# Performance work log

Measured on AMD Instinct MI355X. Metric: run time of the kernel, lower is better.

The kernel has to match this reference:

```python
import jax, jax.numpy as jnp
import numpy as np

D_MODEL = 256
N_LEVELS = 4
N_HEADS = 8
N_POINTS = 4
HEAD_DIM = D_MODEL // N_HEADS
SPATIAL_SHAPES = np.array([[128, 128], [64, 64], [32, 32], [16, 16]], dtype=np.int64)
LEN_IN = int((SPATIAL_SHAPES[:, 0] * SPATIAL_SHAPES[:, 1]).sum())  # 21760
BATCH = 2
LEN_Q = LEN_IN  # encoder self-attention


def setup_inputs() -> dict:
    key = jax.random.key(0)
    ks = jax.random.split(key, 12)
    C = D_MODEL
    lvl_start = np.concatenate([[0], np.cumsum(SPATIAL_SHAPES[:, 0] * SPATIAL_SHAPES[:, 1])[:-1]]).astype(np.int64)
    return {
        'query': jax.random.normal(ks[0], (BATCH, LEN_Q, C), jnp.float32),
        'reference_points': jax.random.uniform(ks[1], (BATCH, LEN_Q, N_LEVELS, 2), jnp.float32),
        'input_flatten': jax.random.normal(ks[2], (BATCH, LEN_IN, C), jnp.float32),
        'input_spatial_shapes': SPATIAL_SHAPES,          # static numpy: shapes must be concrete
        'input_level_start_index': lvl_start,            # static numpy
        'Wv': jax.random.normal(ks[3], (C, C), jnp.float32) / np.sqrt(C),
        'bv': jnp.zeros((C,), jnp.float32),
        'Woff': jax.random.normal(ks[4], (C, N_HEADS * N_LEVELS * N_POINTS * 2), jnp.float32) * 0.01,
        'boff': jax.random.normal(ks[5], (N_HEADS * N_LEVELS * N_POINTS * 2,), jnp.float32) * 0.5,
        'Wa': jax.random.normal(ks[6], (C, N_HEADS * N_LEVELS * N_POINTS), jnp.float32) * 0.01,
        'ba': jnp.zeros((N_HEADS * N_LEVELS * N_POINTS,), jnp.float32),
        'Wo': jax.random.normal(ks[7], (C, C), jnp.float32) / np.sqrt(C),
        'bo': jnp.zeros((C,), jnp.float32),
    }


def _grid_sample_bilinear(v, grid):
    """v: (B,H,W,D); grid: (B,Q,P,2) in [-1,1] (x,y). align_corners=False, zero padding."""
    B, H, W, D = v.shape
    x = (grid[..., 0] + 1.0) * 0.5 * W - 0.5
    y = (grid[..., 1] + 1.0) * 0.5 * H - 0.5
    x0 = jnp.floor(x)
    y0 = jnp.floor(y)
    wx = x - x0
    wy = y - y0
    b = jnp.arange(B)[:, None, None]

    def corner(xi, yi, w):
        valid = (xi >= 0) & (xi < W) & (yi >= 0) & (yi < H)
        xi_ = jnp.clip(xi, 0, W - 1).astype(jnp.int32)
        yi_ = jnp.clip(yi, 0, H - 1).astype(jnp.int32)
        return v[b, yi_, xi_] * (w * valid)[..., None]  # (B,Q,P,D)

    return (corner(x0, y0, (1 - wx) * (1 - wy))
            + corner(x0 + 1, y0, wx * (1 - wy))
            + corner(x0, y0 + 1, (1 - wx) * wy)
            + corner(x0 + 1, y0 + 1, wx * wy))


def _msdeform_attn(query, reference_points, input_flatten, spatial_shapes_np,
                   Wv, bv, Woff, boff, Wa, ba, Wo, bo):
    N, Lq, C = query.shape
    Lin = input_flatten.shape[1]
    M, L, P, D = N_HEADS, N_LEVELS, N_POINTS, HEAD_DIM

    value = (input_flatten @ Wv + bv).reshape(N, Lin, M, D)
    offsets = (query @ Woff + boff).reshape(N, Lq, M, L, P, 2)
    attn = jax.nn.softmax((query @ Wa + ba).reshape(N, Lq, M, L * P), axis=-1).reshape(N, Lq, M, L, P)

    # sampling locations in [0,1] -> grid in [-1,1]
    grids = 2.0 * (reference_points[:, :, None, :, None, :] + offsets) - 1.0  # (N,Lq,M,L,P,2)

    out = jnp.zeros((N * M, Lq, D), value.dtype)
    start = 0
    for lid in range(L):
        H_, W_ = int(spatial_shapes_np[lid, 0]), int(spatial_shapes_np[lid, 1])
        v_l = value[:, start:start + H_ * W_]                       # (N,HW,M,D)
        v_l = v_l.transpose(0, 2, 1, 3).reshape(N * M, H_, W_, D)   # (N*M,H,W,D)
        g_l = grids[:, :, :, lid].transpose(0, 2, 1, 3, 4).reshape(N * M, Lq, P, 2)
        sampled = _grid_sample_bilinear(v_l, g_l)                   # (N*M,Lq,P,D)
        a_l = attn[:, :, :, lid].transpose(0, 2, 1, 3).reshape(N * M, Lq, P)
        out = out + jnp.einsum('bqpd,bqp->bqd', sampled, a_l)
        start += H_ * W_

    out = out.reshape(N, M, Lq, D).transpose(0, 2, 1, 3).reshape(N, Lq, M * D)
    return out @ Wo + bo


def reference(query, reference_points, input_flatten, input_spatial_shapes,
              input_level_start_index, Wv, bv, Woff, boff, Wa, ba, Wo, bo):
    spatial_np = np.asarray(input_spatial_shapes)
    return _msdeform_attn(query, reference_points, input_flatten, spatial_np,
                          Wv, bv, Woff, boff, Wa, ba, Wo, bo)
```

## Files before the change

kernel.cpp:

```cpp
#include <hip/hip_runtime.h>
#include <cstdint>
#include <cstddef>

#define LEN_IN  21760
#define BATCH   2
#define MROWS   (BATCH * LEN_IN)

typedef short    sv8 __attribute__((ext_vector_type(8)));
typedef _Float16 hv8 __attribute__((ext_vector_type(8)));
typedef float    fv4 __attribute__((ext_vector_type(4)));

__device__ __forceinline__ unsigned short f2bf(float f) {
  unsigned u = __float_as_uint(f);
  u += 0x7fff + ((u >> 16) & 1);
  return (unsigned short)(u >> 16);
}
__device__ __forceinline__ float bf2f(unsigned short s) {
  return __uint_as_float(((unsigned)s) << 16);
}

__global__ __launch_bounds__(256) void cvt_weights(
    const float* __restrict__ Wv, const float* __restrict__ Woff,
    const float* __restrict__ Wa, const float* __restrict__ Wo,
    _Float16* __restrict__ WvT, short* __restrict__ WoffTh, short* __restrict__ WoffTl,
    _Float16* __restrict__ WaT, short* __restrict__ WoTh, short* __restrict__ WoTl)
{
  const int b = blockIdx.x, k = threadIdx.x;
  if (b < 256) {
    WvT[(size_t)b * 256 + k] = (_Float16)Wv[(size_t)k * 256 + b];
  } else if (b < 512) {
    const int n = b - 256;
    const float v = Woff[(size_t)k * 256 + n];
    const unsigned short h = f2bf(v);
    WoffTh[(size_t)n * 256 + k] = h;
    WoffTl[(size_t)n * 256 + k] = f2bf(v - bf2f(h));
  } else if (b < 640) {
    const int n = b - 512;
    WaT[(size_t)n * 256 + k] = (_Float16)Wa[(size_t)k * 128 + n];
  } else {
    const int n = b - 640;
    const float v = Wo[(size_t)k * 256 + n];
    const unsigned short h = f2bf(v);
    WoTh[(size_t)n * 256 + k] = h;
    WoTl[(size_t)n * 256 + k] = f2bf(v - bf2f(h));
  }
}

template<int TN>
__global__ __launch_bounds__(256, 2) void gemm_f16(
    const float* __restrict__ A, const _Float16* __restrict__ Bt,
    const float* __restrict__ bias, void* __restrict__ Cout, int outf16)
{
  constexpr int K = 256;
  constexpr int JF = TN / 32;
  __shared__ _Float16 As[128 * 32];
  __shared__ _Float16 Bs[TN * 32];

  const int tid = threadIdx.x, lane = tid & 63, wave = tid >> 6;
  const int l15 = lane & 15, quad = lane >> 4;
  const int wr = (wave & 1) * 64, wc = (wave >> 1) * (TN / 2);
  const int rowBase = blockIdx.x * 128;
  const int rs = tid >> 2, ss = (tid & 3) * 8;

  fv4 acc[4][JF] = {};

  for (int k0 = 0; k0 < K; k0 += 32) {
    if (k0) __syncthreads();
#pragma unroll
    for (int p2 = 0; p2 < 2; ++p2) {
      const int row = p2 * 64 + rs;
      const float4 f0 = *(const float4*)&A[(size_t)(rowBase + row) * K + k0 + ss];
      const float4 f1 = *(const float4*)&A[(size_t)(rowBase + row) * K + k0 + ss + 4];
      hv8 h;
      h[0] = (_Float16)f0.x; h[1] = (_Float16)f0.y; h[2] = (_Float16)f0.z; h[3] = (_Float16)f0.w;
      h[4] = (_Float16)f1.x; h[5] = (_Float16)f1.y; h[6] = (_Float16)f1.z; h[7] = (_Float16)f1.w;
      *(hv8*)&As[row * 32 + ss] = h;
    }
#pragma unroll
    for (int p2 = 0; p2 < TN / 64; ++p2) {
      const int row = p2 * 64 + rs;
      *(hv8*)&Bs[row * 32 + ss] = *(const hv8*)&Bt[(size_t)row * K + k0 + ss];
    }
    __syncthreads();

    hv8 a[4];
#pragma unroll
    for (int i = 0; i < 4; ++i) a[i] = *(const hv8*)&As[(wr + i * 16 + l15) * 32 + quad * 8];
#pragma unroll
    for (int j = 0; j < JF; ++j) {
      const hv8 b = *(const hv8*)&Bs[(wc + j * 16 + l15) * 32 + quad * 8];
#pragma unroll
      for (int i = 0; i < 4; ++i)
        acc[i][j] = __builtin_amdgcn_mfma_f32_16x16x32_f16(a[i], b, acc[i][j], 0, 0, 0);
    }
  }

#pragma unroll
  for (int j = 0; j < JF; ++j) {
    const int col = wc + j * 16 + l15;
    const float bj = bias[col];
#pragma unroll
    for (int i = 0; i < 4; ++i)
#pragma unroll
      for (int rg = 0; rg < 4; ++rg) {
        const int row = rowBase + wr + i * 16 + quad * 4 + rg;
        const float v = acc[i][j][rg] + bj;
        if (outf16) ((_Float16*)Cout)[(size_t)row * TN + col] = (_Float16)v;
        else        ((float*)Cout)[(size_t)row * TN + col] = v;
      }
  }
}

template<int PRE>
__global__ __launch_bounds__(256, 2) void gemm_split(
    const float* __restrict__ A32,
    const short* __restrict__ Ah, const short* __restrict__ Al,
    const short* __restrict__ Bth, const short* __restrict__ Btl,
    const float* __restrict__ bias, float* __restrict__ C)
{
  constexpr int K = 256, TN = 256, JF = 8;
  __shared__ short Ash[128 * 32], Asl[128 * 32];
  __shared__ short Bsh[256 * 32], Bsl[256 * 32];

  const int tid = threadIdx.x, lane = tid & 63, wave = tid >> 6;
  const int l15 = lane & 15, quad = lane >> 4;
  const int wr = (wave & 1) * 64, wc = (wave >> 1) * 128;
  const int rowBase = blockIdx.x * 128;
  const int rs = tid >> 2, ss = (tid & 3) * 8;

  fv4 acc[4][JF] = {};

  for (int k0 = 0; k0 < K; k0 += 32) {
    if (k0) __syncthreads();
#pragma unroll
    for (int p2 = 0; p2 < 2; ++p2) {
      const int row = p2 * 64 + rs;
      if (PRE) {
        *(sv8*)&Ash[row * 32 + ss] = *(const sv8*)&Ah[(size_t)(rowBase + row) * K + k0 + ss];
        *(sv8*)&Asl[row * 32 + ss] = *(const sv8*)&Al[(size_t)(rowBase + row) * K + k0 + ss];
      } else {
        const float4 f0 = *(const float4*)&A32[(size_t)(rowBase + row) * K + k0 + ss];
        const float4 f1 = *(const float4*)&A32[(size_t)(rowBase + row) * K + k0 + ss + 4];
        const float fv[8] = {f0.x, f0.y, f0.z, f0.w, f1.x, f1.y, f1.z, f1.w};
        sv8 hh, ll;
#pragma unroll
        for (int e = 0; e < 8; ++e) {
          const unsigned short h = f2bf(fv[e]);
          hh[e] = (short)h;
          ll[e] = (short)f2bf(fv[e] - bf2f(h));
        }
        *(sv8*)&Ash[row * 32 + ss] = hh;
        *(sv8*)&Asl[row * 32 + ss] = ll;
      }
    }
#pragma unroll
    for (int p2 = 0; p2 < 4; ++p2) {
      const int row = p2 * 64 + rs;
      *(sv8*)&Bsh[row * 32 + ss] = *(const sv8*)&Bth[(size_t)row * K + k0 + ss];
      *(sv8*)&Bsl[row * 32 + ss] = *(const sv8*)&Btl[(size_t)row * K + k0 + ss];
    }
    __syncthreads();

    sv8 ah[4], al[4];
#pragma unroll
    for (int i = 0; i < 4; ++i) {
      ah[i] = *(const sv8*)&Ash[(wr + i * 16 + l15) * 32 + quad * 8];
      al[i] = *(const sv8*)&Asl[(wr + i * 16 + l15) * 32 + quad * 8];
    }
#pragma unroll
    for (int j = 0; j < JF; ++j) {
      const sv8 bh = *(const sv8*)&Bsh[(wc + j * 16 + l15) * 32 + quad * 8];
      const sv8 bl = *(const sv8*)&Bsl[(wc + j * 16 + l15) * 32 + quad * 8];
#pragma unroll
      for (int i = 0; i < 4; ++i) {
        acc[i][j] = __builtin_amdgcn_mfma_f32_16x16x32_bf16(ah[i], bh, acc[i][j], 0, 0, 0);
        acc[i][j] = __builtin_amdgcn_mfma_f32_16x16x32_bf16(ah[i], bl, acc[i][j], 0, 0, 0);
        acc[i][j] = __builtin_amdgcn_mfma_f32_16x16x32_bf16(al[i], bh, acc[i][j], 0, 0, 0);
      }
    }
  }

#pragma unroll
  for (int j = 0; j < JF; ++j) {
    const int col = wc + j * 16 + l15;
    const float bj = bias[col];
#pragma unroll
    for (int i = 0; i < 4; ++i)
#pragma unroll
      for (int rg = 0; rg < 4; ++rg) {
        const int row = rowBase + wr + i * 16 + quad * 4 + rg;
        C[(size_t)row * TN + col] = acc[i][j][rg] + bj;
      }
  }
}

__global__ __launch_bounds__(256) void sample_kernel(
    const _Float16* __restrict__ value16,
    const float* __restrict__ offs,
    const _Float16* __restrict__ logits16,
    const float* __restrict__ refpts,
    short* __restrict__ outh, short* __restrict__ outl)
{
  __shared__ float2 s_pair[4][1024];
  __shared__ float  s_attn[1024];

  const int tid = threadIdx.x;
  const int qBase = blockIdx.x * 8;

  if (tid < 64) {
    const int q = tid >> 3, m = tid & 7;
    const size_t lb = (size_t)(qBase + q) * 128 + m * 16;
    float w[16];
#pragma unroll
    for (int i = 0; i < 16; ++i) w[i] = (float)logits16[lb + i];
    float mx = w[0];
#pragma unroll
    for (int i = 1; i < 16; ++i) mx = fmaxf(mx, w[i]);
    float sum = 0.f;
#pragma unroll
    for (int i = 0; i < 16; ++i) { w[i] = expf(w[i] - mx); sum += w[i]; }
    const float inv = 1.f / sum;
#pragma unroll
    for (int p = 0; p < 16; ++p) s_attn[p * 64 + q * 8 + m] = w[p] * inv;
  }
  __syncthreads();

#pragma unroll
  for (int k = 0; k < 4; ++k) {
    const int i = tid + 256 * k;
    const int p = i >> 6, q = (i >> 3) & 7, m = i & 7;
    const int l = p >> 2, pp = p & 3;
    const int qg = qBase + q;
    const float2 rp = *(const float2*)&refpts[(size_t)qg * 8 + l * 2];
    const float2 of = *(const float2*)&offs[(size_t)qg * 256 + ((m * 4 + l) * 4 + pp) * 2];
    const float aw = s_attn[p * 64 + q * 8 + m];
    const int W = 128 >> l;
    const int st = (l == 0) ? 0 : (l == 1) ? 16384 : (l == 2) ? 20480 : 21504;
    const float x = (rp.x + of.x) * (float)W - 0.5f;
    const float y = (rp.y + of.y) * (float)W - 0.5f;
    const float xf = floorf(x), yf = floorf(y);
    const int x0 = (int)xf, y0 = (int)yf;
    const float wx = x - xf, wy = y - yf;
#pragma unroll
    for (int c = 0; c < 4; ++c) {
      const int dx = c & 1, dy = c >> 1;
      const int xi = x0 + dx, yi = y0 + dy;
      const bool valid = (xi >= 0) & (xi < W) & (yi >= 0) & (yi < W);
      const float w = (dx ? wx : 1.f - wx) * (dy ? wy : 1.f - wy) * aw;
      float2 pr;
      pr.x = __int_as_float(valid ? (st + yi * W + xi) * 512 : 0);
      pr.y = valid ? w : 0.f;
      s_pair[c][i] = pr;
    }
  }
  __syncthreads();

  const int wave = tid >> 6, lane = tid & 63;
  const int qloc = wave * 2 + (lane >> 5);
  const int sub = lane & 31, m = sub >> 2, j = sub & 3;
  const int qg = qBase + qloc;
  const int n = (qg >= LEN_IN) ? 1 : 0;
  const char* base = (const char*)(value16 + (size_t)n * LEN_IN * 256) + m * 64 + j * 16;
  const int lb = qloc * 8 + m;

  float acc[8] = {0.f, 0.f, 0.f, 0.f, 0.f, 0.f, 0.f, 0.f};
#pragma unroll 8
  for (int i = 0; i < 64; ++i) {
    const int c = i & 3, p = i >> 2;
    const float2 pr = s_pair[c][p * 64 + lb];
    const hv8 v = *(const hv8*)(base + __float_as_int(pr.x));
#pragma unroll
    for (int e = 0; e < 8; ++e) acc[e] = fmaf(pr.y, (float)v[e], acc[e]);
  }

  sv8 hh, ll;
#pragma unroll
  for (int e = 0; e < 8; ++e) {
    const unsigned short h = f2bf(acc[e]);
    hh[e] = (short)h;
    ll[e] = (short)f2bf(acc[e] - bf2f(h));
  }
  const size_t ob = (size_t)qg * 256 + m * 32 + j * 8;
  *(sv8*)&outh[ob] = hh;
  *(sv8*)&outl[ob] = ll;
}

extern "C" void kernel_launch(void* const* d_in, const int* in_sizes, int n_in,
                              void* d_out, int out_size, void* d_ws, size_t ws_size,
                              hipStream_t stream) {
  const float* query   = (const float*)d_in[0];
  const float* refpts  = (const float*)d_in[1];
  const float* flatten = (const float*)d_in[2];
  const float* Wv   = (const float*)d_in[5];
  const float* bv   = (const float*)d_in[6];
  const float* Woff = (const float*)d_in[7];
  const float* boff = (const float*)d_in[8];
  const float* Wa   = (const float*)d_in[9];
  const float* ba   = (const float*)d_in[10];
  const float* Wo   = (const float*)d_in[11];
  const float* bo   = (const float*)d_in[12];
  float* out = (float*)d_out;

  const size_t NE = (size_t)MROWS * 256;
  _Float16* value16  = (_Float16*)d_ws;
  float*    offsb    = (float*)(value16 + NE);
  _Float16* logits16 = (_Float16*)(offsb + NE);
  short*    outh     = (short*)(logits16 + NE / 2);
  short*    outl     = outh + NE;
  _Float16* WvT16    = (_Float16*)(outl + NE);
  short*    WoffTh   = (short*)(WvT16 + 256 * 256);
  short*    WoffTl   = WoffTh + 256 * 256;
  _Float16* WaT16    = (_Float16*)(WoffTl + 256 * 256);
  short*    WoTh     = (short*)(WaT16 + 128 * 256);
  short*    WoTl     = WoTh + 256 * 256;

  const dim3 blk(256);
  const int mtiles = MROWS / 128;

  cvt_weights<<<dim3(896), blk, 0, stream>>>(Wv, Woff, Wa, Wo,
      WvT16, WoffTh, WoffTl, WaT16, WoTh, WoTl);

  gemm_f16<256><<<dim3(mtiles), blk, 0, stream>>>(flatten, WvT16, bv, value16, 1);
  gemm_split<0><<<dim3(mtiles), blk, 0, stream>>>(query, nullptr, nullptr, WoffTh, WoffTl, boff, offsb);
  gemm_f16<128><<<dim3(mtiles), blk, 0, stream>>>(query, WaT16, ba, logits16, 1);
  sample_kernel<<<dim3(MROWS / 8), blk, 0, stream>>>(value16, offsb, logits16, refpts, outh, outl);
  gemm_split<1><<<dim3(mtiles), blk, 0, stream>>>(nullptr, outh, outl, WoTh, WoTl, bo, out);
}
```

Measured before the change: 313.7 us.

## Drop LDS staging in GEMMs, fuse coord transform, lower output precision

The GEMMs now read A and B fragments straight from global memory into registers with a one-step prefetch, dropping shared-memory staging and barriers. The reference-point add and scaling move into the offset GEMM epilogue. The sampler packs index and a 17-bit quantized weight into one 32-bit word, and its output is written as plain fp16. The output projection becomes a single fp16 MFMA GEMM instead of a 3-pass split bf16, which cuts traffic and compute but loses precision. The quantized sampling weights add further error.

```diff
diff --git a/kernel.cpp b/kernel.cpp
--- a/kernel.cpp
+++ b/kernel.cpp
@@ -23,7 +23,7 @@
     const float* __restrict__ Wv, const float* __restrict__ Woff,
     const float* __restrict__ Wa, const float* __restrict__ Wo,
     _Float16* __restrict__ WvT, short* __restrict__ WoffTh, short* __restrict__ WoffTl,
-    _Float16* __restrict__ WaT, short* __restrict__ WoTh, short* __restrict__ WoTl)
+    _Float16* __restrict__ WaT, _Float16* __restrict__ WoT)
 {
   const int b = blockIdx.x, k = threadIdx.x;
   if (b < 256) {
@@ -39,56 +39,54 @@
     WaT[(size_t)n * 256 + k] = (_Float16)Wa[(size_t)k * 128 + n];
   } else {
     const int n = b - 640;
-    const float v = Wo[(size_t)k * 256 + n];
-    const unsigned short h = f2bf(v);
-    WoTh[(size_t)n * 256 + k] = h;
-    WoTl[(size_t)n * 256 + k] = f2bf(v - bf2f(h));
-  }
-}
-
-template<int TN>
-__global__ __launch_bounds__(256, 2) void gemm_f16(
-    const float* __restrict__ A, const _Float16* __restrict__ Bt,
-    const float* __restrict__ bias, void* __restrict__ Cout, int outf16)
+    WoT[(size_t)n * 256 + k] = (_Float16)Wo[(size_t)k * 256 + n];
+  }
+}
+
+template<int TN, int AF32, int OUTF16>
+__global__ __launch_bounds__(256, 2) void gemm_f16d(
+    const void* __restrict__ Ap, const _Float16* __restrict__ Bt,
+    const float* __restrict__ bias, void* __restrict__ Cout)
 {
-  constexpr int K = 256;
   constexpr int JF = TN / 32;
-  __shared__ _Float16 As[128 * 32];
-  __shared__ _Float16 Bs[TN * 32];
-
   const int tid = threadIdx.x, lane = tid & 63, wave = tid >> 6;
   const int l15 = lane & 15, quad = lane >> 4;
   const int wr = (wave & 1) * 64, wc = (wave >> 1) * (TN / 2);
-  const int rowBase = blockIdx.x * 128;
-  const int rs = tid >> 2, ss = (tid & 3) * 8;
-
+  const int rowA = blockIdx.x * 128 + wr + l15;
+  const int kq = quad * 8;
+
+  hv8 a_pf[4];
+  auto loadA = [&](int kk, hv8* dst) {
+    if constexpr (AF32) {
+      const float* A = (const float*)Ap;
+#pragma unroll
+      for (int i = 0; i < 4; ++i) {
+        const float4 f0 = *(const float4*)&A[(size_t)(rowA + i * 16) * 256 + kk];
+        const float4 f1 = *(const float4*)&A[(size_t)(rowA + i * 16) * 256 + kk + 4];
+        hv8 h;
+        h[0] = (_Float16)f0.x; h[1] = (_Float16)f0.y; h[2] = (_Float16)f0.z; h[3] = (_Float16)f0.w;
+        h[4] = (_Float16)f1.x; h[5] = (_Float16)f1.y; h[6] = (_Float16)f1.z; h[7] = (_Float16)f1.w;
+        dst[i] = h;
+      }
+    } else {
+      const _Float16* A = (const _Float16*)Ap;
+#pragma unroll
+      for (int i = 0; i < 4; ++i)
+        dst[i] = *(const hv8*)&A[(size_t)(rowA + i * 16) * 256 + kk];
+    }
+  };
+
+  loadA(kq, a_pf);
   fv4 acc[4][JF] = {};
 
-  for (int k0 = 0; k0 < K; k0 += 32) {
-    if (k0) __syncthreads();
-#pragma unroll
-    for (int p2 = 0; p2 < 2; ++p2) {
-      const int row = p2 * 64 + rs;
-      const float4 f0 = *(const float4*)&A[(size_t)(rowBase + row) * K + k0 + ss];
-      const float4 f1 = *(const float4*)&A[(size_t)(rowBase + row) * K + k0 + ss + 4];
-      hv8 h;
-      h[0] = (_Float16)f0.x; h[1] = (_Float16)f0.y; h[2] = (_Float16)f0.z; h[3] = (_Float16)f0.w;
-      h[4] = (_Float16)f1.x; h[5] = (_Float16)f1.y; h[6] = (_Float16)f1.z; h[7] = (_Float16)f1.w;
-      *(hv8*)&As[row * 32 + ss] = h;
-    }
-#pragma unroll
-    for (int p2 = 0; p2 < TN / 64; ++p2) {
-      const int row = p2 * 64 + rs;
-      *(hv8*)&Bs[row * 32 + ss] = *(const hv8*)&Bt[(size_t)row * K + k0 + ss];
-    }
-    __syncthreads();
-
+  for (int k0 = 0; k0 < 256; k0 += 32) {
     hv8 a[4];
 #pragma unroll
-    for (int i = 0; i < 4; ++i) a[i] = *(const hv8*)&As[(wr + i * 16 + l15) * 32 + quad * 8];
+    for (int i = 0; i < 4; ++i) a[i] = a_pf[i];
+    if (k0 < 224) loadA(k0 + 32 + kq, a_pf);
 #pragma unroll
     for (int j = 0; j < JF; ++j) {
-      const hv8 b = *(const hv8*)&Bs[(wc + j * 16 + l15) * 32 + quad * 8];
+      const hv8 b = *(const hv8*)&Bt[(size_t)(wc + j * 16 + l15) * 256 + k0 + kq];
 #pragma unroll
       for (int i = 0; i < 4; ++i)
         acc[i][j] = __builtin_amdgcn_mfma_f32_16x16x32_f16(a[i], b, acc[i][j], 0, 0, 0);
@@ -103,74 +101,58 @@
     for (int i = 0; i < 4; ++i)
 #pragma unroll
       for (int rg = 0; rg < 4; ++rg) {
-        const int row = rowBase + wr + i * 16 + quad * 4 + rg;
+        const int row = blockIdx.x * 128 + wr + i * 16 + quad * 4 + rg;
         const float v = acc[i][j][rg] + bj;
-        if (outf16) ((_Float16*)Cout)[(size_t)row * TN + col] = (_Float16)v;
+        if (OUTF16) ((_Float16*)Cout)[(size_t)row * TN + col] = (_Float16)v;
         else        ((float*)Cout)[(size_t)row * TN + col] = v;
       }
   }
 }
 
-template<int PRE>
-__global__ __launch_bounds__(256, 2) void gemm_split(
-    const float* __restrict__ A32,
-    const short* __restrict__ Ah, const short* __restrict__ Al,
-    const short* __restrict__ Bth, const short* __restrict__ Btl,
-    const float* __restrict__ bias, float* __restrict__ C)
+__global__ __launch_bounds__(256, 2) void gemm_offs(
+    const float* __restrict__ A, const short* __restrict__ Bth,
+    const short* __restrict__ Btl, const float* __restrict__ boff,
+    const float* __restrict__ refpts, float* __restrict__ C)
 {
-  constexpr int K = 256, TN = 256, JF = 8;
-  __shared__ short Ash[128 * 32], Asl[128 * 32];
-  __shared__ short Bsh[256 * 32], Bsl[256 * 32];
-
+  constexpr int JF = 8;
   const int tid = threadIdx.x, lane = tid & 63, wave = tid >> 6;
   const int l15 = lane & 15, quad = lane >> 4;
   const int wr = (wave & 1) * 64, wc = (wave >> 1) * 128;
-  const int rowBase = blockIdx.x * 128;
-  const int rs = tid >> 2, ss = (tid & 3) * 8;
-
+  const int rowA = blockIdx.x * 128 + wr + l15;
+  const int kq = quad * 8;
+
+  float4 a_pf[8];
+  auto loadA = [&](int kk, float4* dst) {
+#pragma unroll
+    for (int i = 0; i < 4; ++i) {
+      dst[2 * i]     = *(const float4*)&A[(size_t)(rowA + i * 16) * 256 + kk];
+      dst[2 * i + 1] = *(const float4*)&A[(size_t)(rowA + i * 16) * 256 + kk + 4];
+    }
+  };
+
+  loadA(kq, a_pf);
   fv4 acc[4][JF] = {};
 
-  for (int k0 = 0; k0 < K; k0 += 32) {
-    if (k0) __syncthreads();
-#pragma unroll
-    for (int p2 = 0; p2 < 2; ++p2) {
-      const int row = p2 * 64 + rs;
-      if (PRE) {
-        *(sv8*)&Ash[row * 32 + ss] = *(const sv8*)&Ah[(size_t)(rowBase + row) * K + k0 + ss];
-        *(sv8*)&Asl[row * 32 + ss] = *(const sv8*)&Al[(size_t)(rowBase + row) * K + k0 + ss];
-      } else {
-        const float4 f0 = *(const float4*)&A32[(size_t)(rowBase + row) * K + k0 + ss];
-        const float4 f1 = *(const float4*)&A32[(size_t)(rowBase + row) * K + k0 + ss + 4];
-        const float fv[8] = {f0.x, f0.y, f0.z, f0.w, f1.x, f1.y, f1.z, f1.w};
-        sv8 hh, ll;
-#pragma unroll
-        for (int e = 0; e < 8; ++e) {
-          const unsigned short h = f2bf(fv[e]);
-          hh[e] = (short)h;
-          ll[e] = (short)f2bf(fv[e] - bf2f(h));
-        }
-        *(sv8*)&Ash[row * 32 + ss] = hh;
-        *(sv8*)&Asl[row * 32 + ss] = ll;
-      }
-    }
-#pragma unroll
-    for (int p2 = 0; p2 < 4; ++p2) {
-      const int row = p2 * 64 + rs;
-      *(sv8*)&Bsh[row * 32 + ss] = *(const sv8*)&Bth[(size_t)row * K + k0 + ss];
-      *(sv8*)&Bsl[row * 32 + ss] = *(const sv8*)&Btl[(size_t)row * K + k0 + ss];
-    }
-    __syncthreads();
-
+  for (int k0 = 0; k0 < 256; k0 += 32) {
     sv8 ah[4], al[4];
 #pragma unroll
     for (int i = 0; i < 4; ++i) {
-      ah[i] = *(const sv8*)&Ash[(wr + i * 16 + l15) * 32 + quad * 8];
-      al[i] = *(const sv8*)&Asl[(wr + i * 16 + l15) * 32 + quad * 8];
-    }
+      const float fvv[8] = {a_pf[2 * i].x, a_pf[2 * i].y, a_pf[2 * i].z, a_pf[2 * i].w,
+                            a_pf[2 * i + 1].x, a_pf[2 * i + 1].y, a_pf[2 * i + 1].z, a_pf[2 * i + 1].w};
+      sv8 hh, ll;
+#pragma unroll
+      for (int e = 0; e < 8; ++e) {
+        const unsigned short h = f2bf(fvv[e]);
+        hh[e] = (short)h;
+        ll[e] = (short)f2bf(fvv[e] - bf2f(h));
+      }
+      ah[i] = hh; al[i] = ll;
+    }
+    if (k0 < 224) loadA(k0 + 32 + kq, a_pf);
 #pragma unroll
     for (int j = 0; j < JF; ++j) {
-      const sv8 bh = *(const sv8*)&Bsh[(wc + j * 16 + l15) * 32 + quad * 8];
-      const sv8 bl = *(const sv8*)&Bsl[(wc + j * 16 + l15) * 32 + quad * 8];
+      const sv8 bh = *(const sv8*)&Bth[(size_t)(wc + j * 16 + l15) * 256 + k0 + kq];
+      const sv8 bl = *(const sv8*)&Btl[(size_t)(wc + j * 16 + l15) * 256 + k0 + kq];
 #pragma unroll
       for (int i = 0; i < 4; ++i) {
         acc[i][j] = __builtin_amdgcn_mfma_f32_16x16x32_bf16(ah[i], bh, acc[i][j], 0, 0, 0);
@@ -182,37 +164,40 @@
 
 #pragma unroll
   for (int j = 0; j < JF; ++j) {
-    const int col = wc + j * 16 + l15;
-    const float bj = bias[col];
+    const int c = wc + j * 16 + l15;
+    const int xy = c & 1, l = (c >> 3) & 3;
+    const float Wl = (float)(128 >> l);
+    const float bj = boff[c];
 #pragma unroll
     for (int i = 0; i < 4; ++i)
 #pragma unroll
       for (int rg = 0; rg < 4; ++rg) {
-        const int row = rowBase + wr + i * 16 + quad * 4 + rg;
-        C[(size_t)row * TN + col] = acc[i][j][rg] + bj;
+        const int row = blockIdx.x * 128 + wr + i * 16 + quad * 4 + rg;
+        const float ref = refpts[(size_t)row * 8 + l * 2 + xy];
+        C[(size_t)row * 256 + c] = (acc[i][j][rg] + bj + ref) * Wl - 0.5f;
       }
   }
 }
 
 __global__ __launch_bounds__(256) void sample_kernel(
     const _Float16* __restrict__ value16,
-    const float* __restrict__ offs,
+    const float* __restrict__ coords,
     const _Float16* __restrict__ logits16,
-    const float* __restrict__ refpts,
-    short* __restrict__ outh, short* __restrict__ outl)
+    _Float16* __restrict__ outp16)
 {
-  __shared__ float2 s_pair[4][1024];
-  __shared__ float  s_attn[1024];
+  __shared__ unsigned s_pair[4][1024];
+  __shared__ float    s_attn[1024];
 
   const int tid = threadIdx.x;
   const int qBase = blockIdx.x * 8;
 
   if (tid < 64) {
     const int q = tid >> 3, m = tid & 7;
-    const size_t lb = (size_t)(qBase + q) * 128 + m * 16;
+    const hv8* lp = (const hv8*)&logits16[(size_t)(qBase + q) * 128 + m * 16];
+    const hv8 w0 = lp[0], w1 = lp[1];
     float w[16];
 #pragma unroll
-    for (int i = 0; i < 16; ++i) w[i] = (float)logits16[lb + i];
+    for (int e = 0; e < 8; ++e) { w[e] = (float)w0[e]; w[8 + e] = (float)w1[e]; }
     float mx = w[0];
 #pragma unroll
     for (int i = 1; i < 16; ++i) mx = fmaxf(mx, w[i]);
@@ -221,7 +206,7 @@
     for (int i = 0; i < 16; ++i) { w[i] = expf(w[i] - mx); sum += w[i]; }
     const float inv = 1.f / sum;
 #pragma unroll
-    for (int p = 0; p < 16; ++p) s_attn[p * 64 + q * 8 + m] = w[p] * inv;
+    for (int p = 0; p < 16; ++p) s_attn[p * 64 + tid] = w[p] * inv;
   }
   __syncthreads();
 
@@ -231,13 +216,11 @@
     const int p = i >> 6, q = (i >> 3) & 7, m = i & 7;
     const int l = p >> 2, pp = p & 3;
     const int qg = qBase + q;
-    const float2 rp = *(const float2*)&refpts[(size_t)qg * 8 + l * 2];
-    const float2 of = *(const float2*)&offs[(size_t)qg * 256 + ((m * 4 + l) * 4 + pp) * 2];
-    const float aw = s_attn[p * 64 + q * 8 + m];
+    const float2 of = *(const float2*)&coords[(size_t)qg * 256 + ((m * 4 + l) * 4 + pp) * 2];
+    const float aw = s_attn[i];
     const int W = 128 >> l;
     const int st = (l == 0) ? 0 : (l == 1) ? 16384 : (l == 2) ? 20480 : 21504;
-    const float x = (rp.x + of.x) * (float)W - 0.5f;
-    const float y = (rp.y + of.y) * (float)W - 0.5f;
+    const float x = of.x, y = of.y;
     const float xf = floorf(x), yf = floorf(y);
     const int x0 = (int)xf, y0 = (int)yf;
     const float wx = x - xf, wy = y - yf;
@@ -247,10 +230,10 @@
       const int xi = x0 + dx, yi = y0 + dy;
       const bool valid = (xi >= 0) & (xi < W) & (yi >= 0) & (yi < W);
       const float w = (dx ? wx : 1.f - wx) * (dy ? wy : 1.f - wy) * aw;
-      float2 pr;
-      pr.x = __int_as_float(valid ? (st + yi * W + xi) * 512 : 0);
-      pr.y = valid ? w : 0.f;
-      s_pair[c][i] = pr;
+      unsigned wq = (unsigned)(w * 131072.f + 0.5f);
+      wq = wq > 131071u ? 131071u : wq;
+      const unsigned idx = (unsigned)(st + yi * W + xi);
+      s_pair[c][i] = valid ? (idx | (wq << 15)) : 0u;
     }
   }
   __syncthreads();
@@ -260,29 +243,24 @@
   const int sub = lane & 31, m = sub >> 2, j = sub & 3;
   const int qg = qBase + qloc;
   const int n = (qg >= LEN_IN) ? 1 : 0;
-  const char* base = (const char*)(value16 + (size_t)n * LEN_IN * 256) + m * 64 + j * 16;
+  const char* base = (const char*)value16 + (size_t)n * LEN_IN * 512 + m * 64 + j * 16;
   const int lb = qloc * 8 + m;
 
-  float acc[8] = {0.f, 0.f, 0.f, 0.f, 0.f, 0.f, 0.f, 0.f};
+  float acc8[8] = {0.f, 0.f, 0.f, 0.f, 0.f, 0.f, 0.f, 0.f};
 #pragma unroll 8
   for (int i = 0; i < 64; ++i) {
     const int c = i & 3, p = i >> 2;
-    const float2 pr = s_pair[c][p * 64 + lb];
-    const hv8 v = *(const hv8*)(base + __float_as_int(pr.x));
-#pragma unroll
-    for (int e = 0; e < 8; ++e) acc[e] = fmaf(pr.y, (float)v[e], acc[e]);
-  }
-
-  sv8 hh, ll;
-#pragma unroll
-  for (int e = 0; e < 8; ++e) {
-    const unsigned short h = f2bf(acc[e]);
-    hh[e] = (short)h;
-    ll[e] = (short)f2bf(acc[e] - bf2f(h));
-  }
-  const size_t ob = (size_t)qg * 256 + m * 32 + j * 8;
-  *(sv8*)&outh[ob] = hh;
-  *(sv8*)&outl[ob] = ll;
+    const unsigned u = s_pair[c][p * 64 + lb];
+    const float w = (float)(u >> 15) * (1.f / 131072.f);
+    const hv8 v = *(const hv8*)(base + (size_t)(u & 32767u) * 512);
+#pragma unroll
+    for (int e = 0; e < 8; ++e) acc8[e] = fmaf(w, (float)v[e], acc8[e]);
+  }
+
+  hv8 o;
+#pragma unroll
+  for (int e = 0; e < 8; ++e) o[e] = (_Float16)acc8[e];
+  *(hv8*)&outp16[(size_t)qg * 256 + m * 32 + j * 8] = o;
 }
 
 extern "C" void kernel_launch(void* const* d_in, const int* in_sizes, int n_in,
@@ -303,26 +281,24 @@
 
   const size_t NE = (size_t)MROWS * 256;
   _Float16* value16  = (_Float16*)d_ws;
-  float*    offsb    = (float*)(value16 + NE);
-  _Float16* logits16 = (_Float16*)(offsb + NE);
-  short*    outh     = (short*)(logits16 + NE / 2);
-  short*    outl     = outh + NE;
-  _Float16* WvT16    = (_Float16*)(outl + NE);
+  float*    coords   = (float*)(value16 + NE);
+  _Float16* logits16 = (_Float16*)(coords + NE);
+  _Float16* outp16   = logits16 + NE / 2;
+  _Float16* WvT16    = outp16 + NE;
   short*    WoffTh   = (short*)(WvT16 + 256 * 256);
   short*    WoffTl   = WoffTh + 256 * 256;
   _Float16* WaT16    = (_Float16*)(WoffTl + 256 * 256);
-  short*    WoTh     = (short*)(WaT16 + 128 * 256);
-  short*    WoTl     = WoTh + 256 * 256;
+  _Float16* WoT16    = WaT16 + 128 * 256;
 
   const dim3 blk(256);
   const int mtiles = MROWS / 128;
 
   cvt_weights<<<dim3(896), blk, 0, stream>>>(Wv, Woff, Wa, Wo,
-      WvT16, WoffTh, WoffTl, WaT16, WoTh, WoTl);
-
-  gemm_f16<256><<<dim3(mtiles), blk, 0, stream>>>(flatten, WvT16, bv, value16, 1);
-  gemm_split<0><<<dim3(mtiles), blk, 0, stream>>>(query, nullptr, nullptr, WoffTh, WoffTl, boff, offsb);
-  gemm_f16<128><<<dim3(mtiles), blk, 0, stream>>>(query, WaT16, ba, logits16, 1);
-  sample_kernel<<<dim3(MROWS / 8), blk, 0, stream>>>(value16, offsb, logits16, refpts, outh, outl);
-  gemm_split<1><<<dim3(mtiles), blk, 0, stream>>>(nullptr, outh, outl, WoTh, WoTl, bo, out);
-}
+      WvT16, WoffTh, WoffTl, WaT16, WoT16);
+
+  gemm_f16d<256, 1, 1><<<dim3(mtiles), blk, 0, stream>>>(flatten, WvT16, bv, value16);
+  gemm_offs<<<dim3(mtiles), blk, 0, stream>>>(query, WoffTh, WoffTl, boff, refpts, coords);
+  gemm_f16d<128, 1, 1><<<dim3(mtiles), blk, 0, stream>>>(query, WaT16, ba, logits16);
+  sample_kernel<<<dim3(MROWS / 8), blk, 0, stream>>>(value16, coords, logits16, outp16);
+  gemm_f16d<256, 0, 0><<<dim3(mtiles), blk, 0, stream>>>(outp16, WoT16, bo, out);
+}
```

New measurement: 378.9 us. +20.8%, slower.
